# Optimization experiments

Hardware: AMD Instinct MI355X
Metric: run time of the kernel (lower is better)

The kernel has to match this reference:

```python
import jax, jax.numpy as jnp
import numpy as np

CHANNEL = 8
K_DIM = 16
D = CHANNEL * K_DIM
ROUT_IT = 3
TAU = 1.0
EPS = 1e-12  # torch F.normalize default


def _normalize(v):
    # L2 normalize over last dim, matching torch.nn.functional.normalize
    nrm = jnp.sqrt(jnp.sum(v * v, axis=-1, keepdims=True))
    return v / jnp.maximum(nrm, EPS)


def setup_inputs() -> dict:
    key = jax.random.key(0)
    k1, k2, k3, k4 = jax.random.split(key, 4)
    n, m = 50000, 32
    in_dim = D  # in_caps * k_dim = 8*16
    x = jax.random.normal(k1, (n, in_dim), dtype=jnp.float32)
    stdv = 1.0 / np.sqrt(float(in_dim))
    W = jax.random.uniform(k2, (D, in_dim), dtype=jnp.float32, minval=-stdv, maxval=stdv)
    b = jax.random.uniform(k3, (D,), dtype=jnp.float32, minval=-stdv, maxval=stdv)
    neighbor_id = jax.random.randint(k4, (n * m,), 0, n + 1, dtype=jnp.int64)
    return {"x": x, "W": W, "b": b, "neighbor_id": neighbor_id}


def reference(x, W, b, neighbor_id):
    n = x.shape[0]
    m = neighbor_id.shape[0] // n
    # fc + relu
    x = jax.nn.relu(x @ W.T + b)
    # per-capsule normalize
    x = _normalize(x.reshape(n, CHANNEL, K_DIM)).reshape(n, D)
    # append zero row for padded neighbor ids, gather neighbors
    z = jnp.concatenate([x, jnp.zeros((1, D), dtype=x.dtype)], axis=0)
    neighbors = z[neighbor_id].reshape(n, m, CHANNEL, K_DIM)
    x_caps = x.reshape(n, CHANNEL, K_DIM)
    u = x_caps
    for it in range(ROUT_IT):
        # agreement logits per (node, neighbor, channel)
        p = jnp.einsum('nck,nmck->nmc', u, neighbors)
        p = jax.nn.softmax(p / TAU, axis=-1)  # softmax over channels
        u = jnp.einsum('nmc,nmck->nck', p, neighbors) + x_caps
        if it < ROUT_IT - 1:
            u = _normalize(u)
    return u.reshape(n, D)
```

## Files before the change

kernel.cpp:

```cpp
#include <hip/hip_runtime.h>
#include <math.h>

#define CHANNEL 8
#define KDIM 16
#define DFULL 128
#define MNBR 32
#define ROUT_IT 3
#define TM1 64
#define NBS 20

typedef __attribute__((ext_vector_type(4))) float f32x4;
typedef __attribute__((ext_vector_type(8))) short short8;
typedef __attribute__((ext_vector_type(8))) _Float16 half8;
typedef __attribute__((ext_vector_type(2))) _Float16 half2v;

__device__ inline unsigned pk16(float a, float b) {
  auto r = __builtin_amdgcn_cvt_pkrtz(a, b);
  return __builtin_bit_cast(unsigned, r);
}
__device__ inline float fdot2(unsigned a, unsigned b, float c) {
  return __builtin_amdgcn_fdot2(__builtin_bit_cast(half2v, a),
                                __builtin_bit_cast(half2v, b), c, false);
}
__device__ inline float h2f_lo(unsigned w) {
  union { ushort u; _Float16 h; } v; v.u = (ushort)(w & 0xffffu); return (float)v.h;
}
__device__ inline float h2f_hi(unsigned w) {
  union { ushort u; _Float16 h; } v; v.u = (ushort)(w >> 16); return (float)v.h;
}
template <int C>
__device__ inline float dppadd(float x) {
  int m = __builtin_amdgcn_update_dpp(0, __builtin_bit_cast(int, x), C, 0xF, 0xF, true);
  return x + __builtin_bit_cast(float, m);
}
__device__ inline float dppswap1(float x) {
  int m = __builtin_amdgcn_update_dpp(0, __builtin_bit_cast(int, x), 0xB1, 0xF, 0xF, true);
  return __builtin_bit_cast(float, m);
}

union H8 { unsigned u[4]; short8 v; };
__device__ inline short8 pack8h(float4 a, float4 b) {
  H8 r;
  r.u[0] = pk16(a.x, a.y); r.u[1] = pk16(a.z, a.w);
  r.u[2] = pk16(b.x, b.y); r.u[3] = pk16(b.z, b.w);
  return r.v;
}

__global__ __launch_bounds__(256) void wpack_kernel(const float* __restrict__ W,
                                                    ushort* __restrict__ wpk) {
  int task = blockIdx.x * 256 + threadIdx.x;
  if (task >= 2048) return;
  int f = task >> 6, l = task & 63;
  int kk = f >> 3, j = f & 7, L = l & 15, H = l >> 4;
  const float* src = W + (size_t)(j * 16 + L) * 128 + kk * 32 + H * 8;
  float4 a = *(const float4*)src;
  float4 b = *(const float4*)(src + 4);
  *(short8*)(wpk + (size_t)task * 8) = pack8h(a, b);
}

__global__ __launch_bounds__(256) void fc_mfma_kernel(
    const float* __restrict__ x, const ushort* __restrict__ wpk,
    const float* __restrict__ bias, ushort* __restrict__ z16, int n) {
  __shared__ __align__(16) float smem[TM1 * 132];

  const int t = threadIdx.x, lane = t & 63, w = t >> 6;

  {
    const uint4* gw = (const uint4*)wpk;
    uint4* lw = (uint4*)smem;
#pragma unroll
    for (int i = 0; i < 8; ++i) lw[i * 256 + t] = gw[i * 256 + t];
  }

  const int L = lane & 15, H = lane >> 4;
  const int r0 = blockIdx.x * TM1;
  const int row = r0 + w * 16 + L;
  const bool ok = row < n;
  const float4 z4 = make_float4(0.f, 0.f, 0.f, 0.f);

  const float* xr = x + (size_t)row * DFULL + H * 8;
  short8 af[4];
#pragma unroll
  for (int kk = 0; kk < 4; ++kk) {
    float4 xa = ok ? *(const float4*)(xr + kk * 32) : z4;
    float4 xb = ok ? *(const float4*)(xr + kk * 32 + 4) : z4;
    af[kk] = pack8h(xa, xb);
  }

  f32x4 acc[8];
#pragma unroll
  for (int j = 0; j < 8; ++j) {
    float bv = bias[j * 16 + L];
    acc[j] = (f32x4){bv, bv, bv, bv};
  }
  __syncthreads();
  const short8* wf = (const short8*)smem;
#pragma unroll
  for (int j = 0; j < 8; ++j)
#pragma unroll
    for (int kk = 0; kk < 4; ++kk) {
      short8 bfr = wf[(kk * 8 + j) * 64 + lane];
      acc[j] = __builtin_amdgcn_mfma_f32_16x16x32_f16(
          __builtin_bit_cast(half8, af[kk]), __builtin_bit_cast(half8, bfr),
          acc[j], 0, 0, 0);
    }
  __syncthreads();

  float* ys = smem;
  const int lr = w * 16 + H * 4;
#pragma unroll
  for (int j = 0; j < 8; ++j)
#pragma unroll
    for (int r = 0; r < 4; ++r)
      ys[(lr + r) * 132 + j * 16 + L] = fmaxf(acc[j][r], 0.f);
  __syncthreads();

#pragma unroll
  for (int pass = 0; pass < 2; ++pass) {
    int task = t + pass * 256;
    int rr = task >> 3, cc = task & 7;
    const float4* yr = (const float4*)(ys + rr * 132 + cc * 16);
    float4 a = yr[0], b = yr[1], c4 = yr[2], d4 = yr[3];
    float ss = a.x * a.x;
    ss = fmaf(a.y, a.y, ss); ss = fmaf(a.z, a.z, ss); ss = fmaf(a.w, a.w, ss);
    ss = fmaf(b.x, b.x, ss); ss = fmaf(b.y, b.y, ss); ss = fmaf(b.z, b.z, ss);
    ss = fmaf(b.w, b.w, ss); ss = fmaf(c4.x, c4.x, ss); ss = fmaf(c4.y, c4.y, ss);
    ss = fmaf(c4.z, c4.z, ss); ss = fmaf(c4.w, c4.w, ss); ss = fmaf(d4.x, d4.x, ss);
    ss = fmaf(d4.y, d4.y, ss); ss = fmaf(d4.z, d4.z, ss); ss = fmaf(d4.w, d4.w, ss);
    float sc = 1.f / fmaxf(sqrtf(ss), 1e-12f);
    int grow = r0 + rr;
    if (grow < n) {
      uint4 o0, o1;
      o0.x = pk16(a.x * sc, a.y * sc);  o0.y = pk16(a.z * sc, a.w * sc);
      o0.z = pk16(b.x * sc, b.y * sc);  o0.w = pk16(b.z * sc, b.w * sc);
      o1.x = pk16(c4.x * sc, c4.y * sc); o1.y = pk16(c4.z * sc, c4.w * sc);
      o1.z = pk16(d4.x * sc, d4.y * sc); o1.w = pk16(d4.z * sc, d4.w * sc);
      uint4* dst = (uint4*)(z16 + (size_t)grow * DFULL + cc * 16);
      dst[0] = o0; dst[1] = o1;
    } else if (grow == n) {
      uint4 zz = {0u, 0u, 0u, 0u};
      uint4* dst = (uint4*)(z16 + (size_t)grow * DFULL + cc * 16);
      dst[0] = zz; dst[1] = zz;
    }
  }
}

__global__ __launch_bounds__(128, 3) void routing_kernel(
    const ushort* __restrict__ z16, const int* __restrict__ nid,
    float* __restrict__ out, int n) {
  __shared__ __align__(16) unsigned nbT[2][DFULL * NBS];
  __shared__ __align__(16) unsigned slT[2][CHANNEL * NBS];
  __shared__ __align__(16) unsigned ulk[2][64];

  const int t = threadIdx.x;
  const int wv = t >> 6, lane = t & 63;
  const int node = blockIdx.x * 2 + wv;
  const int q = lane >> 3, c = lane & 7;
  const int cu = lane >> 4;

  int4 ids = *(const int4*)(nid + node * MNBR + 4 * q);
  const uint4* g0 = (const uint4*)(z16 + (size_t)ids.x * DFULL + c * KDIM);
  const uint4* g1 = (const uint4*)(z16 + (size_t)ids.y * DFULL + c * KDIM);
  const uint4* g2 = (const uint4*)(z16 + (size_t)ids.z * DFULL + c * KDIM);
  const uint4* g3 = (const uint4*)(z16 + (size_t)ids.w * DFULL + c * KDIM);
  uint4 R0a = g0[0], R0b = g0[1];
  uint4 R1a = g1[0], R1b = g1[1];
  uint4 R2a = g2[0], R2b = g2[1];
  uint4 R3a = g3[0], R3b = g3[1];

  const unsigned* zdw = (const unsigned*)z16;
  ulk[wv][lane] = zdw[(size_t)node * 64 + lane];
  unsigned xw0 = zdw[(size_t)node * 64 + (lane >> 1)];
  unsigned xw1 = zdw[(size_t)node * 64 + 32 + (lane >> 1)];
  const float xk0 = (lane & 1) ? h2f_hi(xw0) : h2f_lo(xw0);
  const float xk1 = (lane & 1) ? h2f_hi(xw1) : h2f_lo(xw1);

  unsigned r0[8] = {R0a.x, R0a.y, R0a.z, R0a.w, R0b.x, R0b.y, R0b.z, R0b.w};
  unsigned r1[8] = {R1a.x, R1a.y, R1a.z, R1a.w, R1b.x, R1b.y, R1b.z, R1b.w};
  unsigned r2[8] = {R2a.x, R2a.y, R2a.z, R2a.w, R2b.x, R2b.y, R2b.z, R2b.w};
  unsigned r3[8] = {R3a.x, R3a.y, R3a.z, R3a.w, R3b.x, R3b.y, R3b.z, R3b.w};

  {
    unsigned* nb = nbT[wv];
    const int sl0 = (2 * q + 4 * c) & 15;
    const int sl1 = (2 * q + 1 + 4 * c) & 15;
#pragma unroll
    for (int i = 0; i < 8; ++i) {
      unsigned ev0 = __builtin_amdgcn_perm(r1[i], r0[i], 0x05040100u);
      unsigned od0 = __builtin_amdgcn_perm(r1[i], r0[i], 0x07060302u);
      unsigned ev1 = __builtin_amdgcn_perm(r3[i], r2[i], 0x05040100u);
      unsigned od1 = __builtin_amdgcn_perm(r3[i], r2[i], 0x07060302u);
      nb[(c * KDIM + 2 * i) * NBS + sl0] = ev0;
      nb[(c * KDIM + 2 * i + 1) * NBS + sl0] = od0;
      nb[(c * KDIM + 2 * i) * NBS + sl1] = ev1;
      nb[(c * KDIM + 2 * i + 1) * NBS + sl1] = od1;
    }
  }
  asm volatile("s_waitcnt lgkmcnt(0)" ::: "memory");

  const unsigned* colA = nbT[wv] + lane * NBS;
  const unsigned* colB = nbT[wv] + (lane + 64) * NBS;
  const uint4 nA0 = *(const uint4*)(colA + 0);
  const uint4 nA1 = *(const uint4*)(colA + 4);
  const uint4 nA2 = *(const uint4*)(colA + 8);
  const uint4 nA3 = *(const uint4*)(colA + 12);
  const uint4 nB0 = *(const uint4*)(colB + 0);
  const uint4 nB1 = *(const uint4*)(colB + 4);
  const uint4 nB2 = *(const uint4*)(colB + 8);
  const uint4 nB3 = *(const uint4*)(colB + 12);

  const uint4* upk = (const uint4*)(ulk[wv] + c * 8);
  const int o0 = 4 * ((0 - cu) & 3), o1 = 4 * ((1 - cu) & 3),
            o2 = 4 * ((2 - cu) & 3), o3 = 4 * ((3 - cu) & 3);
  const unsigned* sA = slT[wv] + cu * NBS;
  const unsigned* sB = slT[wv] + (cu + 4) * NBS;
  uint2* swr = (uint2*)(slT[wv]) + c * (NBS / 2) + q;

#pragma unroll
  for (int it = 0; it < ROUT_IT; ++it) {
    {
      uint4 ua = upk[0], ub = upk[1];
      float A0 = 0.f, A1 = 0.f, A2 = 0.f, A3 = 0.f;
      A0 = fdot2(r0[0], ua.x, A0); A1 = fdot2(r1[0], ua.x, A1);
      A2 = fdot2(r2[0], ua.x, A2); A3 = fdot2(r3[0], ua.x, A3);
      A0 = fdot2(r0[1], ua.y, A0); A1 = fdot2(r1[1], ua.y, A1);
      A2 = fdot2(r2[1], ua.y, A2); A3 = fdot2(r3[1], ua.y, A3);
      A0 = fdot2(r0[2], ua.z, A0); A1 = fdot2(r1[2], ua.z, A1);
      A2 = fdot2(r2[2], ua.z, A2); A3 = fdot2(r3[2], ua.z, A3);
      A0 = fdot2(r0[3], ua.w, A0); A1 = fdot2(r1[3], ua.w, A1);
      A2 = fdot2(r2[3], ua.w, A2); A3 = fdot2(r3[3], ua.w, A3);
      A0 = fdot2(r0[4], ub.x, A0); A1 = fdot2(r1[4], ub.x, A1);
      A2 = fdot2(r2[4], ub.x, A2); A3 = fdot2(r3[4], ub.x, A3);
      A0 = fdot2(r0[5], ub.y, A0); A1 = fdot2(r1[5], ub.y, A1);
      A2 = fdot2(r2[5], ub.y, A2); A3 = fdot2(r3[5], ub.y, A3);
      A0 = fdot2(r0[6], ub.z, A0); A1 = fdot2(r1[6], ub.z, A1);
      A2 = fdot2(r2[6], ub.z, A2); A3 = fdot2(r3[6], ub.z, A3);
      A0 = fdot2(r0[7], ub.w, A0); A1 = fdot2(r1[7], ub.w, A1);
      A2 = fdot2(r2[7], ub.w, A2); A3 = fdot2(r3[7], ub.w, A3);
      float e0 = __expf(A0), e1 = __expf(A1), e2 = __expf(A2), e3 = __expf(A3);
      float D0 = dppadd<0x141>(dppadd<0x4E>(dppadd<0xB1>(e0)));
      float D1 = dppadd<0x141>(dppadd<0x4E>(dppadd<0xB1>(e1)));
      float D2 = dppadd<0x141>(dppadd<0x4E>(dppadd<0xB1>(e2)));
      float D3 = dppadd<0x141>(dppadd<0x4E>(dppadd<0xB1>(e3)));
      float s0 = e0 * __builtin_amdgcn_rcpf(D0);
      float s1 = e1 * __builtin_amdgcn_rcpf(D1);
      float s2 = e2 * __builtin_amdgcn_rcpf(D2);
      float s3 = e3 * __builtin_amdgcn_rcpf(D3);
      uint2 sw; sw.x = pk16(s0, s1); sw.y = pk16(s2, s3);
      *swr = sw;
    }
    asm volatile("s_waitcnt lgkmcnt(0)" ::: "memory");
    {
      uint4 v;
      float a = xk0, b = 0.f;
      v = *(const uint4*)(sA + o0);
      a = fdot2(nA0.x, v.x, a); b = fdot2(nA0.y, v.y, b);
      a = fdot2(nA0.z, v.z, a); b = fdot2(nA0.w, v.w, b);
      v = *(const uint4*)(sA + o1);
      a = fdot2(nA1.x, v.x, a); b = fdot2(nA1.y, v.y, b);
      a = fdot2(nA1.z, v.z, a); b = fdot2(nA1.w, v.w, b);
      v = *(const uint4*)(sA + o2);
      a = fdot2(nA2.x, v.x, a); b = fdot2(nA2.y, v.y, b);
      a = fdot2(nA2.z, v.z, a); b = fdot2(nA2.w, v.w, b);
      v = *(const uint4*)(sA + o3);
      a = fdot2(nA3.x, v.x, a); b = fdot2(nA3.y, v.y, b);
      a = fdot2(nA3.z, v.z, a); b = fdot2(nA3.w, v.w, b);
      float u0 = a + b;
      float e = xk1, f = 0.f;
      v = *(const uint4*)(sB + o0);
      e = fdot2(nB0.x, v.x, e); f = fdot2(nB0.y, v.y, f);
      e = fdot2(nB0.z, v.z, e); f = fdot2(nB0.w, v.w, f);
      v = *(const uint4*)(sB + o1);
      e = fdot2(nB1.x, v.x, e); f = fdot2(nB1.y, v.y, f);
      e = fdot2(nB1.z, v.z, e); f = fdot2(nB1.w, v.w, f);
      v = *(const uint4*)(sB + o2);
      e = fdot2(nB2.x, v.x, e); f = fdot2(nB2.y, v.y, f);
      e = fdot2(nB2.z, v.z, e); f = fdot2(nB2.w, v.w, f);
      v = *(const uint4*)(sB + o3);
      e = fdot2(nB3.x, v.x, e); f = fdot2(nB3.y, v.y, f);
      e = fdot2(nB3.z, v.z, e); f = fdot2(nB3.w, v.w, f);
      float u1 = e + f;
      if (it == ROUT_IT - 1) {
        out[(size_t)node * DFULL + lane] = u0;
        out[(size_t)node * DFULL + 64 + lane] = u1;
      } else {
        float ss0 = u0 * u0;
        ss0 = dppadd<0xB1>(ss0); ss0 = dppadd<0x4E>(ss0);
        ss0 = dppadd<0x141>(ss0); ss0 = dppadd<0x140>(ss0);
        float ss1 = u1 * u1;
        ss1 = dppadd<0xB1>(ss1); ss1 = dppadd<0x4E>(ss1);
        ss1 = dppadd<0x141>(ss1); ss1 = dppadd<0x140>(ss1);
        float sc0 = __builtin_amdgcn_rsqf(fmaxf(ss0, 1e-24f));
        float sc1 = __builtin_amdgcn_rsqf(fmaxf(ss1, 1e-24f));
        float un0 = u0 * sc0, un1 = u1 * sc1;
        float p0 = dppswap1(un0), p1 = dppswap1(un1);
        if (!(lane & 1)) {
          ulk[wv][lane >> 1] = pk16(un0, p0);
          ulk[wv][32 + (lane >> 1)] = pk16(un1, p1);
        }
      }
    }
    asm volatile("s_waitcnt lgkmcnt(0)" ::: "memory");
  }
}

extern "C" void kernel_launch(void* const* d_in, const int* in_sizes, int n_in,
                              void* d_out, int out_size, void* d_ws, size_t ws_size,
                              hipStream_t stream) {
  const float* x = (const float*)d_in[0];
  const float* W = (const float*)d_in[1];
  const float* b = (const float*)d_in[2];
  const int* nid = (const int*)d_in[3];
  float* out = (float*)d_out;

  int n = in_sizes[0] / DFULL;
  int g1 = (n + 1 + TM1 - 1) / TM1;
  size_t zrows = (size_t)g1 * TM1;

  ushort* z16 = (ushort*)d_ws;
  ushort* wpk = (ushort*)d_ws + zrows * DFULL;

  wpack_kernel<<<8, 256, 0, stream>>>(W, wpk);
  fc_mfma_kernel<<<g1, 256, 0, stream>>>(x, wpk, b, z16, n);
  routing_kernel<<<n / 2, 128, 0, stream>>>(z16, nid, out, n);
}
```

Before: 149.6 us.

## Replace LDS transpose in routing with register-resident packed-half cross-lane reductions

The routing kernel no longer transposes neighbor data through shared memory. The weighted neighbor sum is now done in registers with packed fp16 FMAs, followed by ds_swizzle and shfl_xor butterfly reductions across the neighbor lanes. Normalisation runs per lane on replicated capsule data, and blocks grow to four waves with a bounds check. This removes LDS traffic and waitcnt stalls and raises occupancy, but accumulating in fp16 instead of fp32 risks a loss of accuracy.

```diff
diff --git a/kernel.cpp b/kernel.cpp
--- a/kernel.cpp
+++ b/kernel.cpp
@@ -7,7 +7,6 @@
 #define MNBR 32
 #define ROUT_IT 3
 #define TM1 64
-#define NBS 20
 
 typedef __attribute__((ext_vector_type(4))) float f32x4;
 typedef __attribute__((ext_vector_type(8))) short short8;
@@ -28,14 +27,15 @@
 __device__ inline float h2f_hi(unsigned w) {
   union { ushort u; _Float16 h; } v; v.u = (ushort)(w >> 16); return (float)v.h;
 }
+__device__ inline half2v h2(unsigned u) { return __builtin_bit_cast(half2v, u); }
+__device__ inline unsigned unh(half2v h) { return __builtin_bit_cast(unsigned, h); }
+__device__ inline unsigned pkfma16(unsigned a, unsigned b, unsigned c) {
+  return unh(__builtin_elementwise_fma(h2(a), h2(b), h2(c)));
+}
 template <int C>
 __device__ inline float dppadd(float x) {
   int m = __builtin_amdgcn_update_dpp(0, __builtin_bit_cast(int, x), C, 0xF, 0xF, true);
   return x + __builtin_bit_cast(float, m);
-}
-__device__ inline float dppswap1(float x) {
-  int m = __builtin_amdgcn_update_dpp(0, __builtin_bit_cast(int, x), 0xB1, 0xF, 0xF, true);
-  return __builtin_bit_cast(float, m);
 }
 
 union H8 { unsigned u[4]; short8 v; };
@@ -145,18 +145,14 @@
   }
 }
 
-__global__ __launch_bounds__(128, 3) void routing_kernel(
+__global__ __launch_bounds__(256, 4) void routing_kernel(
     const ushort* __restrict__ z16, const int* __restrict__ nid,
     float* __restrict__ out, int n) {
-  __shared__ __align__(16) unsigned nbT[2][DFULL * NBS];
-  __shared__ __align__(16) unsigned slT[2][CHANNEL * NBS];
-  __shared__ __align__(16) unsigned ulk[2][64];
-
   const int t = threadIdx.x;
-  const int wv = t >> 6, lane = t & 63;
-  const int node = blockIdx.x * 2 + wv;
+  const int node = blockIdx.x * 4 + (t >> 6);
+  if (node >= n) return;
+  const int lane = t & 63;
   const int q = lane >> 3, c = lane & 7;
-  const int cu = lane >> 4;
 
   int4 ids = *(const int4*)(nid + node * MNBR + 4 * q);
   const uint4* g0 = (const uint4*)(z16 + (size_t)ids.x * DFULL + c * KDIM);
@@ -167,140 +163,87 @@
   uint4 R1a = g1[0], R1b = g1[1];
   uint4 R2a = g2[0], R2b = g2[1];
   uint4 R3a = g3[0], R3b = g3[1];
-
-  const unsigned* zdw = (const unsigned*)z16;
-  ulk[wv][lane] = zdw[(size_t)node * 64 + lane];
-  unsigned xw0 = zdw[(size_t)node * 64 + (lane >> 1)];
-  unsigned xw1 = zdw[(size_t)node * 64 + 32 + (lane >> 1)];
-  const float xk0 = (lane & 1) ? h2f_hi(xw0) : h2f_lo(xw0);
-  const float xk1 = (lane & 1) ? h2f_hi(xw1) : h2f_lo(xw1);
-
   unsigned r0[8] = {R0a.x, R0a.y, R0a.z, R0a.w, R0b.x, R0b.y, R0b.z, R0b.w};
   unsigned r1[8] = {R1a.x, R1a.y, R1a.z, R1a.w, R1b.x, R1b.y, R1b.z, R1b.w};
   unsigned r2[8] = {R2a.x, R2a.y, R2a.z, R2a.w, R2b.x, R2b.y, R2b.z, R2b.w};
   unsigned r3[8] = {R3a.x, R3a.y, R3a.z, R3a.w, R3b.x, R3b.y, R3b.z, R3b.w};
 
-  {
-    unsigned* nb = nbT[wv];
-    const int sl0 = (2 * q + 4 * c) & 15;
-    const int sl1 = (2 * q + 1 + 4 * c) & 15;
-#pragma unroll
-    for (int i = 0; i < 8; ++i) {
-      unsigned ev0 = __builtin_amdgcn_perm(r1[i], r0[i], 0x05040100u);
-      unsigned od0 = __builtin_amdgcn_perm(r1[i], r0[i], 0x07060302u);
-      unsigned ev1 = __builtin_amdgcn_perm(r3[i], r2[i], 0x05040100u);
-      unsigned od1 = __builtin_amdgcn_perm(r3[i], r2[i], 0x07060302u);
-      nb[(c * KDIM + 2 * i) * NBS + sl0] = ev0;
-      nb[(c * KDIM + 2 * i + 1) * NBS + sl0] = od0;
-      nb[(c * KDIM + 2 * i) * NBS + sl1] = ev1;
-      nb[(c * KDIM + 2 * i + 1) * NBS + sl1] = od1;
-    }
-  }
-  asm volatile("s_waitcnt lgkmcnt(0)" ::: "memory");
-
-  const unsigned* colA = nbT[wv] + lane * NBS;
-  const unsigned* colB = nbT[wv] + (lane + 64) * NBS;
-  const uint4 nA0 = *(const uint4*)(colA + 0);
-  const uint4 nA1 = *(const uint4*)(colA + 4);
-  const uint4 nA2 = *(const uint4*)(colA + 8);
-  const uint4 nA3 = *(const uint4*)(colA + 12);
-  const uint4 nB0 = *(const uint4*)(colB + 0);
-  const uint4 nB1 = *(const uint4*)(colB + 4);
-  const uint4 nB2 = *(const uint4*)(colB + 8);
-  const uint4 nB3 = *(const uint4*)(colB + 12);
-
-  const uint4* upk = (const uint4*)(ulk[wv] + c * 8);
-  const int o0 = 4 * ((0 - cu) & 3), o1 = 4 * ((1 - cu) & 3),
-            o2 = 4 * ((2 - cu) & 3), o3 = 4 * ((3 - cu) & 3);
-  const unsigned* sA = slT[wv] + cu * NBS;
-  const unsigned* sB = slT[wv] + (cu + 4) * NBS;
-  uint2* swr = (uint2*)(slT[wv]) + c * (NBS / 2) + q;
+  const uint4* xp = (const uint4*)(z16 + (size_t)node * DFULL + c * KDIM);
+  uint4 X0 = xp[0], X1 = xp[1];
+  unsigned xpk[8] = {X0.x, X0.y, X0.z, X0.w, X1.x, X1.y, X1.z, X1.w};
+  unsigned upk[8];
+#pragma unroll
+  for (int i = 0; i < 8; ++i) upk[i] = xpk[i];
 
 #pragma unroll
   for (int it = 0; it < ROUT_IT; ++it) {
+    float A0 = 0.f, A1 = 0.f, A2 = 0.f, A3 = 0.f;
+#pragma unroll
+    for (int i = 0; i < 8; ++i) {
+      A0 = fdot2(r0[i], upk[i], A0);
+      A1 = fdot2(r1[i], upk[i], A1);
+      A2 = fdot2(r2[i], upk[i], A2);
+      A3 = fdot2(r3[i], upk[i], A3);
+    }
+    float e0 = __expf(A0), e1 = __expf(A1), e2 = __expf(A2), e3 = __expf(A3);
+    float D0 = dppadd<0x141>(dppadd<0x4E>(dppadd<0xB1>(e0)));
+    float D1 = dppadd<0x141>(dppadd<0x4E>(dppadd<0xB1>(e1)));
+    float D2 = dppadd<0x141>(dppadd<0x4E>(dppadd<0xB1>(e2)));
+    float D3 = dppadd<0x141>(dppadd<0x4E>(dppadd<0xB1>(e3)));
+    unsigned sp0, sp1, sp2, sp3;
     {
-      uint4 ua = upk[0], ub = upk[1];
-      float A0 = 0.f, A1 = 0.f, A2 = 0.f, A3 = 0.f;
-      A0 = fdot2(r0[0], ua.x, A0); A1 = fdot2(r1[0], ua.x, A1);
-      A2 = fdot2(r2[0], ua.x, A2); A3 = fdot2(r3[0], ua.x, A3);
-      A0 = fdot2(r0[1], ua.y, A0); A1 = fdot2(r1[1], ua.y, A1);
-      A2 = fdot2(r2[1], ua.y, A2); A3 = fdot2(r3[1], ua.y, A3);
-      A0 = fdot2(r0[2], ua.z, A0); A1 = fdot2(r1[2], ua.z, A1);
-      A2 = fdot2(r2[2], ua.z, A2); A3 = fdot2(r3[2], ua.z, A3);
-      A0 = fdot2(r0[3], ua.w, A0); A1 = fdot2(r1[3], ua.w, A1);
-      A2 = fdot2(r2[3], ua.w, A2); A3 = fdot2(r3[3], ua.w, A3);
-      A0 = fdot2(r0[4], ub.x, A0); A1 = fdot2(r1[4], ub.x, A1);
-      A2 = fdot2(r2[4], ub.x, A2); A3 = fdot2(r3[4], ub.x, A3);
-      A0 = fdot2(r0[5], ub.y, A0); A1 = fdot2(r1[5], ub.y, A1);
-      A2 = fdot2(r2[5], ub.y, A2); A3 = fdot2(r3[5], ub.y, A3);
-      A0 = fdot2(r0[6], ub.z, A0); A1 = fdot2(r1[6], ub.z, A1);
-      A2 = fdot2(r2[6], ub.z, A2); A3 = fdot2(r3[6], ub.z, A3);
-      A0 = fdot2(r0[7], ub.w, A0); A1 = fdot2(r1[7], ub.w, A1);
-      A2 = fdot2(r2[7], ub.w, A2); A3 = fdot2(r3[7], ub.w, A3);
-      float e0 = __expf(A0), e1 = __expf(A1), e2 = __expf(A2), e3 = __expf(A3);
-      float D0 = dppadd<0x141>(dppadd<0x4E>(dppadd<0xB1>(e0)));
-      float D1 = dppadd<0x141>(dppadd<0x4E>(dppadd<0xB1>(e1)));
-      float D2 = dppadd<0x141>(dppadd<0x4E>(dppadd<0xB1>(e2)));
-      float D3 = dppadd<0x141>(dppadd<0x4E>(dppadd<0xB1>(e3)));
       float s0 = e0 * __builtin_amdgcn_rcpf(D0);
       float s1 = e1 * __builtin_amdgcn_rcpf(D1);
       float s2 = e2 * __builtin_amdgcn_rcpf(D2);
       float s3 = e3 * __builtin_amdgcn_rcpf(D3);
-      uint2 sw; sw.x = pk16(s0, s1); sw.y = pk16(s2, s3);
-      *swr = sw;
-    }
-    asm volatile("s_waitcnt lgkmcnt(0)" ::: "memory");
-    {
-      uint4 v;
-      float a = xk0, b = 0.f;
-      v = *(const uint4*)(sA + o0);
-      a = fdot2(nA0.x, v.x, a); b = fdot2(nA0.y, v.y, b);
-      a = fdot2(nA0.z, v.z, a); b = fdot2(nA0.w, v.w, b);
-      v = *(const uint4*)(sA + o1);
-      a = fdot2(nA1.x, v.x, a); b = fdot2(nA1.y, v.y, b);
-      a = fdot2(nA1.z, v.z, a); b = fdot2(nA1.w, v.w, b);
-      v = *(const uint4*)(sA + o2);
-      a = fdot2(nA2.x, v.x, a); b = fdot2(nA2.y, v.y, b);
-      a = fdot2(nA2.z, v.z, a); b = fdot2(nA2.w, v.w, b);
-      v = *(const uint4*)(sA + o3);
-      a = fdot2(nA3.x, v.x, a); b = fdot2(nA3.y, v.y, b);
-      a = fdot2(nA3.z, v.z, a); b = fdot2(nA3.w, v.w, b);
-      float u0 = a + b;
-      float e = xk1, f = 0.f;
-      v = *(const uint4*)(sB + o0);
-      e = fdot2(nB0.x, v.x, e); f = fdot2(nB0.y, v.y, f);
-      e = fdot2(nB0.z, v.z, e); f = fdot2(nB0.w, v.w, f);
-      v = *(const uint4*)(sB + o1);
-      e = fdot2(nB1.x, v.x, e); f = fdot2(nB1.y, v.y, f);
-      e = fdot2(nB1.z, v.z, e); f = fdot2(nB1.w, v.w, f);
-      v = *(const uint4*)(sB + o2);
-      e = fdot2(nB2.x, v.x, e); f = fdot2(nB2.y, v.y, f);
-      e = fdot2(nB2.z, v.z, e); f = fdot2(nB2.w, v.w, f);
-      v = *(const uint4*)(sB + o3);
-      e = fdot2(nB3.x, v.x, e); f = fdot2(nB3.y, v.y, f);
-      e = fdot2(nB3.z, v.z, e); f = fdot2(nB3.w, v.w, f);
-      float u1 = e + f;
-      if (it == ROUT_IT - 1) {
-        out[(size_t)node * DFULL + lane] = u0;
-        out[(size_t)node * DFULL + 64 + lane] = u1;
-      } else {
-        float ss0 = u0 * u0;
-        ss0 = dppadd<0xB1>(ss0); ss0 = dppadd<0x4E>(ss0);
-        ss0 = dppadd<0x141>(ss0); ss0 = dppadd<0x140>(ss0);
-        float ss1 = u1 * u1;
-        ss1 = dppadd<0xB1>(ss1); ss1 = dppadd<0x4E>(ss1);
-        ss1 = dppadd<0x141>(ss1); ss1 = dppadd<0x140>(ss1);
-        float sc0 = __builtin_amdgcn_rsqf(fmaxf(ss0, 1e-24f));
-        float sc1 = __builtin_amdgcn_rsqf(fmaxf(ss1, 1e-24f));
-        float un0 = u0 * sc0, un1 = u1 * sc1;
-        float p0 = dppswap1(un0), p1 = dppswap1(un1);
-        if (!(lane & 1)) {
-          ulk[wv][lane >> 1] = pk16(un0, p0);
-          ulk[wv][32 + (lane >> 1)] = pk16(un1, p1);
-        }
-      }
-    }
-    asm volatile("s_waitcnt lgkmcnt(0)" ::: "memory");
+      sp0 = pk16(s0, s0); sp1 = pk16(s1, s1);
+      sp2 = pk16(s2, s2); sp3 = pk16(s3, s3);
+    }
+    unsigned acc[8];
+#pragma unroll
+    for (int i = 0; i < 8; ++i) {
+      unsigned a = unh(h2(r3[i]) * h2(sp3));
+      a = pkfma16(r2[i], sp2, a);
+      a = pkfma16(r1[i], sp1, a);
+      acc[i] = pkfma16(r0[i], sp0, a);
+    }
+#pragma unroll
+    for (int i = 0; i < 8; ++i) {
+      int v = __builtin_amdgcn_ds_swizzle((int)acc[i], 0x201F);
+      acc[i] = unh(h2(acc[i]) + h2((unsigned)v));
+    }
+#pragma unroll
+    for (int i = 0; i < 8; ++i) {
+      int v = __builtin_amdgcn_ds_swizzle((int)acc[i], 0x401F);
+      acc[i] = unh(h2(acc[i]) + h2((unsigned)v));
+    }
+#pragma unroll
+    for (int i = 0; i < 8; ++i) {
+      int v = __shfl_xor((int)acc[i], 32);
+      acc[i] = unh(h2(acc[i]) + h2((unsigned)v));
+    }
+#pragma unroll
+    for (int i = 0; i < 8; ++i) acc[i] = unh(h2(acc[i]) + h2(xpk[i]));
+
+    if (it == ROUT_IT - 1) {
+      unsigned a0 = (q & 1) ? acc[1] : acc[0];
+      unsigned a1 = (q & 1) ? acc[3] : acc[2];
+      unsigned a2 = (q & 1) ? acc[5] : acc[4];
+      unsigned a3 = (q & 1) ? acc[7] : acc[6];
+      unsigned b0 = (q & 2) ? a1 : a0;
+      unsigned b1 = (q & 2) ? a3 : a2;
+      unsigned sel = (q & 4) ? b1 : b0;
+      float2 st; st.x = h2f_lo(sel); st.y = h2f_hi(sel);
+      *(float2*)(out + (size_t)node * DFULL + c * KDIM + 2 * q) = st;
+    } else {
+      float ss = 0.f;
+#pragma unroll
+      for (int i = 0; i < 8; ++i) ss = fdot2(acc[i], acc[i], ss);
+      float sc = __builtin_amdgcn_rsqf(fmaxf(ss, 1e-24f));
+      unsigned scp = pk16(sc, sc);
+#pragma unroll
+      for (int i = 0; i < 8; ++i) upk[i] = unh(h2(acc[i]) * h2(scp));
+    }
   }
 }
 
@@ -322,5 +265,5 @@
 
   wpack_kernel<<<8, 256, 0, stream>>>(W, wpk);
   fc_mfma_kernel<<<g1, 256, 0, stream>>>(x, wpk, b, z16, n);
-  routing_kernel<<<n / 2, 128, 0, stream>>>(z16, nid, out, n);
-}
+  routing_kernel<<<(n + 3) / 4, 256, 0, stream>>>(z16, nid, out, n);
+}
```

New measurement: 143.9 us. 1.04x faster.
